# Performance work log

Hardware: AMD Instinct MI355X
Metric: run time of the kernel (lower is better)

The kernel has to match this reference:

```python
import jax, jax.numpy as jnp
import numpy as np


def setup_inputs() -> dict:
    key = jax.random.key(0)
    k1, k2, k3 = jax.random.split(key, 3)
    B, S, H, E = 8, 4096, 2048, 64
    hidden_states = jax.random.normal(k1, (B, S, H), dtype=jnp.float32)
    # kaiming_uniform-ish scale for the gate weight [E, H]
    weight = jax.random.normal(k2, (E, H), dtype=jnp.float32) * (1.0 / np.sqrt(H))
    # load-balancing biases are small perturbations of the softmax scores
    expert_biases = jax.random.normal(k3, (E,), dtype=jnp.float32) * 0.01
    return {"hidden_states": hidden_states, "weight": weight,
            "expert_biases": expert_biases, "top_k": 8}


def reference(hidden_states, weight, expert_biases, top_k):
    B, S, H = hidden_states.shape
    x = hidden_states.reshape(-1, H).astype(jnp.float32)          # [T, H], T = B*S
    logits = jnp.einsum('th,eh->te', x, weight.astype(jnp.float32))  # [T, E]
    scores = jax.nn.softmax(logits, axis=-1)                      # fp32 softmax
    bias_scores = scores + expert_biases[None, :]                 # bias-adjusted routing
    _, topk_indices = jax.lax.top_k(bias_scores, top_k)           # [T, K] (sorted; set equals torch sorted=False)
    topk_weights = jnp.take_along_axis(scores, topk_indices, axis=1)  # gather original probs
    if top_k > 1:  # norm_topk_prob=True
        topk_weights = topk_weights / (topk_weights.sum(-1, keepdims=True) + 1e-20)
    return (topk_indices.astype(jnp.int32),
            topk_weights.astype(hidden_states.dtype))
```

## Files before the change

### kernel.cpp

```cpp
#include <hip/hip_runtime.h>
#include <math.h>

#define Hdim   2048
#define HF4    512
#define MARGIN 2e-5f
#define CAPF   16384
#define PROBE0 1237
#define PROBE1 20011

#define WS_FCNT  0
#define WS_BAD   4
#define WS_PROBE 64
#define WS_FLIST 1024
#define WS_WH    (128*1024)
#define WS_WL    (384*1024)
#define WS_NEED  (640*1024)

typedef float f32x4 __attribute__((ext_vector_type(4)));
typedef short bf8   __attribute__((ext_vector_type(8)));

__device__ __forceinline__ short bf_hi(float v, float& rem) {
  const unsigned u  = __builtin_bit_cast(unsigned, v);
  const unsigned uh = u & 0xffff0000u;
  rem = v - __builtin_bit_cast(float, uh);
  return (short)(u >> 16);
}
__device__ __forceinline__ short bf_rne(float v) {
  const unsigned u = __builtin_bit_cast(unsigned, v);
  return (short)((u + 0x7fffu + ((u >> 16) & 1u)) >> 16);
}

__global__ __launch_bounds__(256) void gate_prep(
    const float* __restrict__ wgt, short* __restrict__ WH, short* __restrict__ WL)
{
  const int f  = blockIdx.x * 256 + threadIdx.x;
  const int c  = f >> 11;
  const int et = (f >> 9) & 3;
  const int l  = (f >> 3) & 63;
  const int j  = f & 7;
  const int e  = et * 16 + (l & 15);
  const int k  = c * 32 + (l >> 4) * 8 + j;
  const float w = wgt[(size_t)e * Hdim + k];
  float r; const short h = bf_hi(w, r);
  WH[f] = h; WL[f] = bf_rne(r);
}

__global__ __launch_bounds__(256, 3) void gate_main(
    const float* __restrict__ x, const short* __restrict__ WH,
    const short* __restrict__ WL, const float* __restrict__ eb,
    float* __restrict__ out, int* __restrict__ fcnt, int* __restrict__ flist,
    float* __restrict__ probelg, int T)
{
  __shared__ float redu[2][64][17];
  const int t  = threadIdx.x;
  const int wv = t >> 6;
  const int tg = wv >> 1;
  const int kh = wv & 1;
  const int ln = t & 63;
  const int tb = blockIdx.x * 32 + tg * 16;

  const char* xq = (const char*)(x + (size_t)(tb + (ln & 15)) * Hdim
                                 + (size_t)kh * 1024 + (ln >> 4) * 8);
  const short* whp = WH;
  const short* wlp = WL;
  const unsigned voff = (unsigned)(ln * 16) + ((unsigned)kh << 17);

  f32x4 acc[4];
  #pragma unroll
  for (int et = 0; et < 4; ++et) acc[et] = (f32x4)0.f;

  f32x4 P0a, P0b, P1a, P1b;
  bf8 WEh0, WEh1, WEh2, WEh3, WEl0, WEl1, WEl2, WEl3;
  bf8 WOh0, WOh1, WOh2, WOh3, WOl0, WOl1, WOl2, WOl3;

#define XLOAD(D0, D1, OA, OB)                                              \
  asm volatile("global_load_dwordx4 %0, %2, off offset:" #OA "\n\t"        \
               "global_load_dwordx4 %1, %2, off offset:" #OB               \
               : "=v"(D0), "=v"(D1) : "v"(xq))

#define WLOAD4(D0,D1,D2,D3, BASE)                                          \
  asm volatile(                                                            \
    "global_load_dwordx4 %0, %4, %5 offset:0\n\t"                          \
    "global_load_dwordx4 %1, %4, %5 offset:1024\n\t"                       \
    "global_load_dwordx4 %2, %4, %5 offset:2048\n\t"                       \
    "global_load_dwordx4 %3, %4, %5 offset:3072"                           \
    : "=v"(D0), "=v"(D1), "=v"(D2), "=v"(D3)                               \
    : "v"(voff), "s"(BASE))

#define WSTG(H0,H1,H2,H3, L0,L1,L2,L3) {                                   \
    WLOAD4(H0,H1,H2,H3, whp);                                              \
    WLOAD4(L0,L1,L2,L3, wlp);                                              \
    whp += 2048; wlp += 2048; }

#define WAITC(VM)                                                          \
  asm volatile("s_waitcnt vmcnt(" #VM ")" ::: "memory");                   \
  __builtin_amdgcn_sched_barrier(0);

#define COMP(XA, XB, H0,H1,H2,H3, L0,L1,L2,L3) {                                  \
    bf8 ah, al;                                                                   \
    _Pragma("unroll")                                                             \
    for (int j = 0; j < 4; ++j) { float r_;                                       \
      ah[j]     = bf_hi(XA[j], r_);  al[j]     = bf_rne(r_);                      \
      ah[j + 4] = bf_hi(XB[j], r_);  al[j + 4] = bf_rne(r_); }                    \
    __builtin_amdgcn_s_setprio(1);                                                \
    acc[0] = __builtin_amdgcn_mfma_f32_16x16x32_bf16(ah, H0, acc[0], 0, 0, 0);    \
    acc[0] = __builtin_amdgcn_mfma_f32_16x16x32_bf16(ah, L0, acc[0], 0, 0, 0);    \
    acc[0] = __builtin_amdgcn_mfma_f32_16x16x32_bf16(al, H0, acc[0], 0, 0, 0);    \
    acc[0] = __builtin_amdgcn_mfma_f32_16x16x32_bf16(al, L0, acc[0], 0, 0, 0);    \
    acc[1] = __builtin_amdgcn_mfma_f32_16x16x32_bf16(ah, H1, acc[1], 0, 0, 0);    \
    acc[1] = __builtin_amdgcn_mfma_f32_16x16x32_bf16(ah, L1, acc[1], 0, 0, 0);    \
    acc[1] = __builtin_amdgcn_mfma_f32_16x16x32_bf16(al, H1, acc[1], 0, 0, 0);    \
    acc[1] = __builtin_amdgcn_mfma_f32_16x16x32_bf16(al, L1, acc[1], 0, 0, 0);    \
    acc[2] = __builtin_amdgcn_mfma_f32_16x16x32_bf16(ah, H2, acc[2], 0, 0, 0);    \
    acc[2] = __builtin_amdgcn_mfma_f32_16x16x32_bf16(ah, L2, acc[2], 0, 0, 0);    \
    acc[2] = __builtin_amdgcn_mfma_f32_16x16x32_bf16(al, H2, acc[2], 0, 0, 0);    \
    acc[2] = __builtin_amdgcn_mfma_f32_16x16x32_bf16(al, L2, acc[2], 0, 0, 0);    \
    acc[3] = __builtin_amdgcn_mfma_f32_16x16x32_bf16(ah, H3, acc[3], 0, 0, 0);    \
    acc[3] = __builtin_amdgcn_mfma_f32_16x16x32_bf16(ah, L3, acc[3], 0, 0, 0);    \
    acc[3] = __builtin_amdgcn_mfma_f32_16x16x32_bf16(al, H3, acc[3], 0, 0, 0);    \
    acc[3] = __builtin_amdgcn_mfma_f32_16x16x32_bf16(al, L3, acc[3], 0, 0, 0);    \
    __builtin_amdgcn_s_setprio(0);                                                \
  }

#define CE(XA,XB) COMP(XA,XB, WEh0,WEh1,WEh2,WEh3, WEl0,WEl1,WEl2,WEl3)
#define CO(XA,XB) COMP(XA,XB, WOh0,WOh1,WOh2,WOh3, WOl0,WOl1,WOl2,WOl3)
#define WE_ WSTG(WEh0,WEh1,WEh2,WEh3, WEl0,WEl1,WEl2,WEl3)
#define WO_ WSTG(WOh0,WOh1,WOh2,WOh3, WOl0,WOl1,WOl2,WOl3)

  WE_;  XLOAD(P0a, P0b, 0,   16);
  WO_;  XLOAD(P1a, P1b, 128, 144);

  #pragma unroll 1
  for (int it = 0; it < 7; ++it) {
    WAITC(10); CE(P0a, P0b); WE_; XLOAD(P0a, P0b, 256, 272);
    WAITC(10); CO(P1a, P1b); WO_; XLOAD(P1a, P1b, 384, 400);
    WAITC(10); CE(P0a, P0b); WE_; XLOAD(P0a, P0b, 512, 528);
    WAITC(10); CO(P1a, P1b); WO_; XLOAD(P1a, P1b, 640, 656);
    xq += 512;
  }
  WAITC(10); CE(P0a, P0b); WE_; XLOAD(P0a, P0b, 256, 272);
  WAITC(10); CO(P1a, P1b); WO_; XLOAD(P1a, P1b, 384, 400);
  WAITC(10); CE(P0a, P0b);
  WAITC(0);  CO(P1a, P1b);
#undef WE_
#undef WO_
#undef CE
#undef CO
#undef COMP
#undef WAITC
#undef WSTG
#undef WLOAD4
#undef XLOAD

  if (kh) {
    #pragma unroll
    for (int et = 0; et < 4; ++et)
      #pragma unroll
      for (int r = 0; r < 4; ++r)
        redu[tg][ln][et * 4 + r] = acc[et][r];
  }
  __syncthreads();
  if (kh) return;
  #pragma unroll
  for (int et = 0; et < 4; ++et)
    #pragma unroll
    for (int r = 0; r < 4; ++r)
      acc[et][r] += redu[tg][ln][et * 4 + r];

  const int c = ln & 15, g = ln >> 4;
  float bias4[4];
  #pragma unroll
  for (int et = 0; et < 4; ++et) bias4[et] = eb[et * 16 + c];

  #pragma unroll
  for (int r = 0; r < 4; ++r) {
    const int gt = tb + g * 4 + r;
    const float z0 = acc[0][r], z1 = acc[1][r], z2 = acc[2][r], z3 = acc[3][r];
    if (gt == PROBE0) { probelg[c]      = z0; probelg[16 + c] = z1;
                        probelg[32 + c] = z2; probelg[48 + c] = z3; }
    if (gt == PROBE1) { probelg[64 + c]  = z0; probelg[80 + c]  = z1;
                        probelg[96 + c]  = z2; probelg[112 + c] = z3; }
    float m = fmaxf(fmaxf(z0, z1), fmaxf(z2, z3));
    #pragma unroll
    for (int off = 1; off < 16; off <<= 1) m = fmaxf(m, __shfl_xor(m, off, 64));
    const float p0 = expf(z0 - m), p1 = expf(z1 - m);
    const float p2 = expf(z2 - m), p3 = expf(z3 - m);
    float Zs = (p0 + p1) + (p2 + p3);
    #pragma unroll
    for (int off = 1; off < 16; off <<= 1) Zs += __shfl_xor(Zs, off, 64);
    const float inv = 1.f / Zs;
    const float s0 = p0 * inv, s1 = p1 * inv, s2 = p2 * inv, s3 = p3 * inv;
    float b0 = s0 + bias4[0], b1 = s1 + bias4[1];
    float b2 = s2 + bias4[2], b3 = s3 + bias4[3];
    float prev = 0.f, gmin = 1e30f, mys = 0.f;
    int myi = 0;
    #pragma unroll
    for (int r9 = 0; r9 < 9; ++r9) {
      float v = b0; int ie = 0;
      if (b1 > v) { v = b1; ie = 1; }
      if (b2 > v) { v = b2; ie = 2; }
      if (b3 > v) { v = b3; ie = 3; }
      int idx = ie * 16 + c;
      #pragma unroll
      for (int off = 1; off < 16; off <<= 1) {
        const float ov = __shfl_xor(v, off, 64);
        const int   oi = __shfl_xor(idx, off, 64);
        if (ov > v || (ov == v && oi < idx)) { v = ov; idx = oi; }
      }
      if (r9) gmin = fminf(gmin, prev - v);
      prev = v;
      if (r9 < 8) {
        const int oe = idx >> 4, oc = idx & 15;
        const float cand = oe == 0 ? s0 : oe == 1 ? s1 : oe == 2 ? s2 : s3;
        const float sv = __shfl(cand, g * 16 + oc, 64);
        if (c == r9) { myi = idx; mys = sv; }
        if (c == oc) {
          if (oe == 0) b0 = -1e30f;
          else if (oe == 1) b1 = -1e30f;
          else if (oe == 2) b2 = -1e30f;
          else b3 = -1e30f;
        }
      }
    }
    float wsum = (c < 8) ? mys : 0.f;
    #pragma unroll
    for (int off = 1; off < 16; off <<= 1) wsum += __shfl_xor(wsum, off, 64);
    if (c < 8) {
      out[(size_t)gt * 8 + c] = (float)myi;
      out[(size_t)T * 8 + (size_t)gt * 8 + c] = mys / (wsum + 1e-20f);
    }
    if (c == 0 && gmin < MARGIN) {
      const int pos = atomicAdd(fcnt, 1);
      if (pos < CAPF) flist[pos] = gt;
    }
  }
}

__global__ __launch_bounds__(256) void gate_check(
    const float* __restrict__ x, const float* __restrict__ wgt,
    const float* __restrict__ probelg, const int* __restrict__ fcnt,
    int* __restrict__ allbad)
{
  __shared__ float part[64][4];
  const int p = blockIdx.x;
  const int P = p ? PROBE1 : PROBE0;
  const int t = threadIdx.x, e = t >> 2, q = t & 3;
  const float4* xr = (const float4*)(x + (size_t)P * Hdim);
  const float4* wr = (const float4*)(wgt + (size_t)e * Hdim);
  float a = 0.f, b = 0.f, c = 0.f, d = 0.f;
  for (int i = 0; i < 128; ++i) {
    const int f4 = i * 4 + q;
    const float4 xv = xr[f4], wv = wr[f4];
    a = fmaf(xv.x, wv.x, a); b = fmaf(xv.y, wv.y, b);
    c = fmaf(xv.z, wv.z, c); d = fmaf(xv.w, wv.w, d);
  }
  part[e][q] = (a + b) + (c + d);
  __syncthreads();
  if (q == 0) {
    const float z = part[e][0] + part[e][1] + part[e][2] + part[e][3];
    if (fabsf(z - probelg[p * 64 + e]) > 0.05f) *allbad = 1;
  }
  if (t == 0 && p == 0 && *fcnt > CAPF) *allbad = 1;
}

__global__ __launch_bounds__(256) void gate_fix(
    const float* __restrict__ x, const float* __restrict__ wgt,
    const float* __restrict__ eb, float* __restrict__ out,
    const int* __restrict__ fcnt, const int* __restrict__ flist,
    const int* __restrict__ allbad, int T)
{
  __shared__ float4 xl[4 * HF4];
  __shared__ double part[4][64][4];
  __shared__ int tks[4];
  const int bad = *allbad;
  int n = bad ? T : *fcnt;
  if (n <= 0) return;
  if (!bad && n > CAPF) n = CAPF;
  const int nb = (n + 3) >> 2;
  const int t = threadIdx.x;
  for (int b = blockIdx.x; b < nb; b += gridDim.x) {
    if (t < 4) {
      const int li = b * 4 + t;
      const int ci = li < n ? li : n - 1;
      tks[t] = bad ? ci : flist[ci];
    }
    __syncthreads();
    {
      const int m = t >> 6, l2 = t & 63;
      const float4* src = (const float4*)x + (size_t)tks[m] * HF4;
      #pragma unroll
      for (int ii = 0; ii < 8; ++ii) xl[m * HF4 + ii * 64 + l2] = src[ii * 64 + l2];
    }
    __syncthreads();
    const int e = t >> 2, q = t & 3;
    double acc[4] = {0.0, 0.0, 0.0, 0.0};
    const float4* w4 = (const float4*)wgt + (size_t)e * HF4;
    for (int c = 0; c < 128; ++c) {
      const int f4 = c * 4 + q;
      const float4 wvv = w4[f4];
      #pragma unroll
      for (int m = 0; m < 4; ++m) {
        const float4 xv = xl[m * HF4 + f4];
        acc[m] += (double)xv.x * (double)wvv.x + (double)xv.y * (double)wvv.y
                + (double)xv.z * (double)wvv.z + (double)xv.w * (double)wvv.w;
      }
    }
    #pragma unroll
    for (int m = 0; m < 4; ++m) part[m][e][q] = acc[m];
    __syncthreads();
    {
      const int m = t >> 6, ln = t & 63;
      const double z = part[m][ln][0] + part[m][ln][1] + part[m][ln][2] + part[m][ln][3];
      double mx = z;
      #pragma unroll
      for (int off = 32; off; off >>= 1) mx = fmax(mx, __shfl_xor(mx, off, 64));
      const double p = exp(z - mx);
      double Zs = p;
      #pragma unroll
      for (int off = 32; off; off >>= 1) Zs += __shfl_xor(Zs, off, 64);
      const double sco = p / Zs;
      double bsw = sco + (double)eb[ln];
      double mys = 0.0;
      int myi = 0;
      #pragma unroll
      for (int r = 0; r < 8; ++r) {
        double v = bsw;
        int idx = ln;
        #pragma unroll
        for (int off = 32; off; off >>= 1) {
          const double ov = __shfl_xor(v, off, 64);
          const int   oi = __shfl_xor(idx, off, 64);
          if (ov > v || (ov == v && oi < idx)) { v = ov; idx = oi; }
        }
        const double sv = __shfl(sco, idx, 64);
        if (ln == r)  { myi = idx; mys = sv; }
        if (ln == idx) bsw = -1.0e300;
      }
      double wsum = (ln < 8) ? mys : 0.0;
      #pragma unroll
      for (int off = 32; off; off >>= 1) wsum += __shfl_xor(wsum, off, 64);
      const int gt = tks[m];
      if (ln < 8) {
        out[(size_t)gt * 8 + ln] = (float)myi;
        out[(size_t)T * 8 + (size_t)gt * 8 + ln] = (float)(mys / (wsum + 1e-20));
      }
    }
    __syncthreads();
  }
}

extern "C" void kernel_launch(void* const* d_in, const int* in_sizes, int n_in,
                              void* d_out, int out_size, void* d_ws, size_t ws_size,
                              hipStream_t stream) {
  const float* x   = (const float*)d_in[0];
  const float* wgt = (const float*)d_in[1];
  const float* eb  = (const float*)d_in[2];
  float* out = (float*)d_out;
  const int T = in_sizes[0] / Hdim;
  char* ws = (char*)d_ws;
  int*   fcnt    = (int*)(ws + WS_FCNT);
  int*   bad     = (int*)(ws + WS_BAD);
  float* probelg = (float*)(ws + WS_PROBE);
  int*   flist   = (int*)(ws + WS_FLIST);
  short* WH      = (short*)(ws + WS_WH);
  short* WL      = (short*)(ws + WS_WL);

  if (ws_size < WS_NEED) {
    (void)hipMemsetAsync(ws, 0, 8, stream);
    (void)hipMemsetAsync(ws + WS_BAD, 1, 1, stream);
    hipLaunchKernelGGL(gate_fix, dim3(256), dim3(256), 0, stream,
                       x, wgt, eb, out, fcnt, flist, bad, T);
    return;
  }
  (void)hipMemsetAsync(ws, 0, 8, stream);
  hipLaunchKernelGGL(gate_prep, dim3(512), dim3(256), 0, stream, wgt, WH, WL);
  hipLaunchKernelGGL(gate_main, dim3(T / 32), dim3(256), 0, stream,
                     x, WH, WL, eb, out, fcnt, flist, probelg, T);
  hipLaunchKernelGGL(gate_check, dim3(2), dim3(256), 0, stream,
                     x, wgt, probelg, fcnt, bad);
  hipLaunchKernelGGL(gate_fix, dim3(256), dim3(256), 0, stream,
                     x, wgt, eb, out, fcnt, flist, bad, T);
}
```

Measured before the change: 166.9 us.

## Stage x tiles into swizzled LDS via direct global-to-LDS loads, drop K-split

The main gate kernel no longer splits K across wave pairs with an LDS reduction. Each wave now owns 16 tokens over the full hidden dimension, and x tiles are staged into double-buffered, XOR-swizzled LDS using global_load_lds 16-byte transfers. Blocks cover 64 tokens instead of 32, and occupancy drops to 2 blocks per CU because of the 64KB shared buffer. The aim is fully coalesced x streaming and no cross-wave reduction or barrier, at the cost of lower occupancy and more complex waitcnt sequencing.

```diff
diff --git a/kernel.cpp b/kernel.cpp
--- a/kernel.cpp
+++ b/kernel.cpp
@@ -18,6 +18,12 @@
 
 typedef float f32x4 __attribute__((ext_vector_type(4)));
 typedef short bf8   __attribute__((ext_vector_type(8)));
+
+typedef const __attribute__((address_space(1))) unsigned int ga_u32;
+typedef __attribute__((address_space(3))) unsigned int la_u32;
+__device__ __forceinline__ void gload16(const void* g, void* l) {
+  __builtin_amdgcn_global_load_lds((ga_u32*)g, (la_u32*)l, 16, 0, 0);
+}
 
 __device__ __forceinline__ short bf_hi(float v, float& rem) {
   const unsigned u  = __builtin_bit_cast(unsigned, v);
@@ -45,38 +51,43 @@
   WH[f] = h; WL[f] = bf_rne(r);
 }
 
-__global__ __launch_bounds__(256, 3) void gate_main(
+__global__ __launch_bounds__(256, 2) void gate_main(
     const float* __restrict__ x, const short* __restrict__ WH,
     const short* __restrict__ WL, const float* __restrict__ eb,
     float* __restrict__ out, int* __restrict__ fcnt, int* __restrict__ flist,
     float* __restrict__ probelg, int T)
 {
-  __shared__ float redu[2][64][17];
+  __shared__ __align__(16) char xbuf[65536];
   const int t  = threadIdx.x;
   const int wv = t >> 6;
-  const int tg = wv >> 1;
-  const int kh = wv & 1;
   const int ln = t & 63;
-  const int tb = blockIdx.x * 32 + tg * 16;
-
-  const char* xq = (const char*)(x + (size_t)(tb + (ln & 15)) * Hdim
-                                 + (size_t)kh * 1024 + (ln >> 4) * 8);
+  const int tb = blockIdx.x * 64 + wv * 16;
+
+  char* wb = xbuf + wv * 16384;
+
+  const int h   = ln >> 5;
+  const int l31 = ln & 31;
+  const char* xrow = (const char*)x + (size_t)(tb + h) * 8192;
+  const unsigned uo0 = (unsigned)((l31 ^ ((0 + h) & 7)) * 16);
+  const unsigned uo1 = (unsigned)((l31 ^ ((2 + h) & 7)) * 16);
+  const unsigned uo2 = (unsigned)((l31 ^ ((4 + h) & 7)) * 16);
+  const unsigned uo3 = (unsigned)((l31 ^ ((6 + h) & 7)) * 16);
+
+  const int t16 = ln & 15, q = ln >> 4;
+  const int swz = t16 & 7;
+  const char* xr0 = wb + t16 * 512 + (((q * 2 + 0) ^ swz) * 16);
+  const char* xr1 = wb + t16 * 512 + (((q * 2 + 1) ^ swz) * 16);
+
   const short* whp = WH;
   const short* wlp = WL;
-  const unsigned voff = (unsigned)(ln * 16) + ((unsigned)kh << 17);
+  const unsigned voff = (unsigned)(ln * 16);
 
   f32x4 acc[4];
   #pragma unroll
   for (int et = 0; et < 4; ++et) acc[et] = (f32x4)0.f;
 
-  f32x4 P0a, P0b, P1a, P1b;
   bf8 WEh0, WEh1, WEh2, WEh3, WEl0, WEl1, WEl2, WEl3;
   bf8 WOh0, WOh1, WOh2, WOh3, WOl0, WOl1, WOl2, WOl3;
-
-#define XLOAD(D0, D1, OA, OB)                                              \
-  asm volatile("global_load_dwordx4 %0, %2, off offset:" #OA "\n\t"        \
-               "global_load_dwordx4 %1, %2, off offset:" #OB               \
-               : "=v"(D0), "=v"(D1) : "v"(xq))
 
 #define WLOAD4(D0,D1,D2,D3, BASE)                                          \
   asm volatile(                                                            \
@@ -84,7 +95,7 @@
     "global_load_dwordx4 %1, %4, %5 offset:1024\n\t"                       \
     "global_load_dwordx4 %2, %4, %5 offset:2048\n\t"                       \
     "global_load_dwordx4 %3, %4, %5 offset:3072"                           \
-    : "=v"(D0), "=v"(D1), "=v"(D2), "=v"(D3)                               \
+    : "=&v"(D0), "=&v"(D1), "=&v"(D2), "=&v"(D3)                           \
     : "v"(voff), "s"(BASE))
 
 #define WSTG(H0,H1,H2,H3, L0,L1,L2,L3) {                                   \
@@ -92,9 +103,25 @@
     WLOAD4(L0,L1,L2,L3, wlp);                                              \
     whp += 2048; wlp += 2048; }
 
+#define WE_ WSTG(WEh0,WEh1,WEh2,WEh3, WEl0,WEl1,WEl2,WEl3)
+#define WO_ WSTG(WOh0,WOh1,WOh2,WOh3, WOl0,WOl1,WOl2,WOl3)
+
 #define WAITC(VM)                                                          \
   asm volatile("s_waitcnt vmcnt(" #VM ")" ::: "memory");                   \
   __builtin_amdgcn_sched_barrier(0);
+
+#define XS(nb) {                                                           \
+    const char* s_ = xrow + (size_t)(nb) * 512;                            \
+    char* d_ = wb + (((nb) & 1) << 13);                                    \
+    gload16(s_ +      0 + uo0, d_ + 0);                                    \
+    gload16(s_ +  16384 + uo1, d_ + 1024);                                 \
+    gload16(s_ +  32768 + uo2, d_ + 2048);                                 \
+    gload16(s_ +  49152 + uo3, d_ + 3072);                                 \
+    gload16(s_ +  65536 + uo0, d_ + 4096);                                 \
+    gload16(s_ +  81920 + uo1, d_ + 5120);                                 \
+    gload16(s_ +  98304 + uo2, d_ + 6144);                                 \
+    gload16(s_ + 114688 + uo3, d_ + 7168);                                 \
+  }
 
 #define COMP(XA, XB, H0,H1,H2,H3, L0,L1,L2,L3) {                                  \
     bf8 ah, al;                                                                   \
@@ -122,50 +149,47 @@
     __builtin_amdgcn_s_setprio(0);                                                \
   }
 
-#define CE(XA,XB) COMP(XA,XB, WEh0,WEh1,WEh2,WEh3, WEl0,WEl1,WEl2,WEl3)
-#define CO(XA,XB) COMP(XA,XB, WOh0,WOh1,WOh2,WOh3, WOl0,WOl1,WOl2,WOl3)
-#define WE_ WSTG(WEh0,WEh1,WEh2,WEh3, WEl0,WEl1,WEl2,WEl3)
-#define WO_ WSTG(WOh0,WOh1,WOh2,WOh3, WOl0,WOl1,WOl2,WOl3)
-
-  WE_;  XLOAD(P0a, P0b, 0,   16);
-  WO_;  XLOAD(P1a, P1b, 128, 144);
+#define STEPE(BO, SS, VM) {                                                \
+    WAITC(VM);                                                             \
+    f32x4 Af0 = *(const f32x4*)(xr0 + (BO) + (SS) * 128);                  \
+    f32x4 Af1 = *(const f32x4*)(xr1 + (BO) + (SS) * 128);                  \
+    COMP(Af0, Af1, WEh0,WEh1,WEh2,WEh3, WEl0,WEl1,WEl2,WEl3);              \
+  }
+#define STEPO(BO, SS, VM) {                                                \
+    WAITC(VM);                                                             \
+    f32x4 Af0 = *(const f32x4*)(xr0 + (BO) + (SS) * 128);                  \
+    f32x4 Af1 = *(const f32x4*)(xr1 + (BO) + (SS) * 128);                  \
+    COMP(Af0, Af1, WOh0,WOh1,WOh2,WOh3, WOl0,WOl1,WOl2,WOl3);              \
+  }
+
+  XS(0);
+  WE_;
+  WO_;
 
   #pragma unroll 1
-  for (int it = 0; it < 7; ++it) {
-    WAITC(10); CE(P0a, P0b); WE_; XLOAD(P0a, P0b, 256, 272);
-    WAITC(10); CO(P1a, P1b); WO_; XLOAD(P1a, P1b, 384, 400);
-    WAITC(10); CE(P0a, P0b); WE_; XLOAD(P0a, P0b, 512, 528);
-    WAITC(10); CO(P1a, P1b); WO_; XLOAD(P1a, P1b, 640, 656);
-    xq += 512;
-  }
-  WAITC(10); CE(P0a, P0b); WE_; XLOAD(P0a, P0b, 256, 272);
-  WAITC(10); CO(P1a, P1b); WO_; XLOAD(P1a, P1b, 384, 400);
-  WAITC(10); CE(P0a, P0b);
-  WAITC(0);  CO(P1a, P1b);
+  for (int c = 0; c < 15; ++c) {
+    const int bo = (c & 1) << 13;
+    asm volatile("s_waitcnt lgkmcnt(0)" ::: "memory");
+    __builtin_amdgcn_sched_barrier(0);
+    XS(c + 1);
+    STEPE(bo, 0, 16); WE_;
+    STEPO(bo, 1, 16); WO_;
+    STEPE(bo, 2, 8);  WE_;
+    STEPO(bo, 3, 8);  WO_;
+  }
+  STEPE(8192, 0, 8); WE_;
+  STEPO(8192, 1, 8); WO_;
+  STEPE(8192, 2, 8);
+  STEPO(8192, 3, 0);
+#undef STEPO
+#undef STEPE
+#undef COMP
+#undef XS
+#undef WAITC
 #undef WE_
 #undef WO_
-#undef CE
-#undef CO
-#undef COMP
-#undef WAITC
 #undef WSTG
 #undef WLOAD4
-#undef XLOAD
-
-  if (kh) {
-    #pragma unroll
-    for (int et = 0; et < 4; ++et)
-      #pragma unroll
-      for (int r = 0; r < 4; ++r)
-        redu[tg][ln][et * 4 + r] = acc[et][r];
-  }
-  __syncthreads();
-  if (kh) return;
-  #pragma unroll
-  for (int et = 0; et < 4; ++et)
-    #pragma unroll
-    for (int r = 0; r < 4; ++r)
-      acc[et][r] += redu[tg][ln][et * 4 + r];
 
   const int c = ln & 15, g = ln >> 4;
   float bias4[4];
@@ -374,7 +398,7 @@
   }
   (void)hipMemsetAsync(ws, 0, 8, stream);
   hipLaunchKernelGGL(gate_prep, dim3(512), dim3(256), 0, stream, wgt, WH, WL);
-  hipLaunchKernelGGL(gate_main, dim3(T / 32), dim3(256), 0, stream,
+  hipLaunchKernelGGL(gate_main, dim3(T / 64), dim3(256), 0, stream,
                      x, WH, WL, eb, out, fcnt, flist, probelg, T);
   hipLaunchKernelGGL(gate_check, dim3(2), dim3(256), 0, stream,
                      x, wgt, probelg, fcnt, bad);
```

New measurement: 159.4 us. 1.05x faster.
